# Optimization experiments

Hardware: AMD Instinct MI355X
Metric: run time of the kernel (lower is better)

The kernel has to match this reference:

```python
import jax, jax.numpy as jnp
import numpy as np

M, K, N, P = 2048, 4096, 64, 16   # prev outputs, decoder nodes, matrix size, parents per node
ACTIVE_THRESHOLD = 12             # >= 12/16 active parents required

def setup_inputs() -> dict:
    key = jax.random.key(0)
    k1, k2, k3, k4, k5 = jax.random.split(key, 5)
    prev_outputs = jax.random.normal(k1, (M, N, N), dtype=jnp.float32)
    prev_is_active = jax.random.bernoulli(k2, 0.9, (M,))                 # bool (M,)
    parent_indices = jax.random.randint(k3, (K, P), 0, M)                # static wiring (K,16)
    w = jax.random.normal(k4, (K, P), dtype=jnp.float32) / np.sqrt(P)    # per-node parent weights
    b = jax.random.normal(k5, (K,), dtype=jnp.float32) * 0.01            # per-node bias
    return {"prev_outputs": prev_outputs, "prev_is_active": prev_is_active,
            "parent_indices": parent_indices, "w": w, "b": b}

def reference(prev_outputs, prev_is_active, parent_indices, w, b):
    # gather parent outputs: (K, P, n, n)
    gathered = prev_outputs[parent_indices]
    # per-node decoder: weighted combine of 16 parents + bias, tanh
    combined = jnp.einsum('kp,kpnm->knm', w, gathered) + b[:, None, None]
    out = jnp.tanh(combined)[:, None]                                    # (K,1,n,n)
    # activity threshold gate: node active iff >= 12 of 16 parents active
    n_active = prev_is_active[parent_indices].astype(jnp.int32).sum(axis=-1)  # (K,)
    out_active = n_active >= ACTIVE_THRESHOLD
    out = jnp.where(out_active[:, None, None, None], out, jnp.zeros_like(out))
    return out, out_active
```

## Files before the change

### kernel.cpp

```cpp
#include <hip/hip_runtime.h>


#define M_ROWS   2048
#define K_NODES  4096
#define NN       4096
#define POS_TILE 16
#define NTHREADS 1024
#define ROW_B    40
#define LDS_BYTES (M_ROWS * ROW_B)
#define OUT_ELEMS (K_NODES * NN)
#define ACTIVE_THRESHOLD 12

typedef float f32x4 __attribute__((ext_vector_type(4)));
typedef unsigned short u16x4 __attribute__((ext_vector_type(4)));

__device__ __forceinline__ float fast_tanh(float x) {
  float ax = __builtin_fabsf(x);
  float e  = __expf(-2.0f * ax);
  float r  = (1.0f - e) * __builtin_amdgcn_rcpf(1.0f + e);
  return __builtin_copysignf(r, x);
}

__device__ __forceinline__ unsigned short f2bf_rne(float f) {
  unsigned u = __float_as_uint(f);
  u += 0x7FFFu + ((u >> 16) & 1u);
  return (unsigned short)(u >> 16);
}

__global__ __launch_bounds__(256) void act_kernel(
    const int* __restrict__ pidx, const unsigned int* __restrict__ isact,
    float* __restrict__ outact) {
  __shared__ int mode_sh;
  if (threadIdx.x == 0) mode_sh = 0;
  __syncthreads();
  int bad = 0;
  for (int i = threadIdx.x; i < 512; i += 256) bad |= (isact[i] > 1u);
  if (bad) atomicOr(&mode_sh, 1);
  __syncthreads();
  const int shift = mode_sh ? 0 : 2;
  const unsigned char* actb = (const unsigned char*)isact;

  int k = blockIdx.x * 256 + threadIdx.x;
  const int4* ip = (const int4*)(pidx + k * 16);
  int4 ia = ip[0], ib = ip[1], ic = ip[2], id4 = ip[3];
  int ids[16] = {ia.x, ia.y, ia.z, ia.w, ib.x, ib.y, ib.z, ib.w,
                 ic.x, ic.y, ic.z, ic.w, id4.x, id4.y, id4.z, id4.w};
  int n = 0;
  #pragma unroll
  for (int p = 0; p < 16; ++p) n += (actb[ids[p] << shift] != 0);
  outact[k] = (n >= ACTIVE_THRESHOLD) ? 1.0f : 0.0f;
}

#define PFMA4(vv, wv)                                             \
  { float wv_ = (wv);                                             \
    a0 += wv_ * __uint_as_float((unsigned)(vv)[0] << 16);         \
    a1 += wv_ * __uint_as_float((unsigned)(vv)[1] << 16);         \
    a2 += wv_ * __uint_as_float((unsigned)(vv)[2] << 16);         \
    a3 += wv_ * __uint_as_float((unsigned)(vv)[3] << 16); }

__global__ __launch_bounds__(NTHREADS, 8) void decoder_kernel(
    const float* __restrict__ prev, const int* __restrict__ pidx,
    const float* __restrict__ w, const float* __restrict__ b,
    const float* __restrict__ actf, float* __restrict__ out) {
  extern __shared__ char xb[];
  const int tid = threadIdx.x;
  const int bid = blockIdx.x;

  const int xcd   = bid & 7;
  const int j     = bid >> 3;
  const int tile  = xcd * 32 + (j >> 1);
  const int half  = j & 1;
  const int pos0  = tile * POS_TILE;
  const int nbase = half * (K_NODES / 2);

  #pragma unroll
  for (int it = 0; it < 8; ++it) {
    int ci = (it << 10) + tid;
    int r = ci >> 2, c = ci & 3;
    f32x4 v = *(const f32x4*)(prev + r * NN + pos0 + (c << 2));
    u16x4 o;
    o[0] = f2bf_rne(v.x); o[1] = f2bf_rne(v.y);
    o[2] = f2bf_rne(v.z); o[3] = f2bf_rne(v.w);
    *(u16x4*)(xb + r * ROW_B + (c << 3)) = o;
  }
  __syncthreads();

  const int q  = tid & 3;
  const int s  = tid >> 2;
  const int qb = q << 3;

  for (int it = 0; it < 8; ++it) {
    int n = nbase + (it << 8) + s;
    const int4*   ip = (const int4*)(pidx + (n << 4));
    const float4* wp = (const float4*)(w + (n << 4));
    float bk = b[n];
    float g  = actf[n];

    float a0 = bk, a1 = bk, a2 = bk, a3 = bk;

    #pragma unroll
    for (int bb = 0; bb < 4; ++bb) {
      int4   iv = ip[bb];
      float4 wv = wp[bb];
      u16x4 v0 = *(const u16x4*)(xb + iv.x * ROW_B + qb);
      u16x4 v1 = *(const u16x4*)(xb + iv.y * ROW_B + qb);
      u16x4 v2 = *(const u16x4*)(xb + iv.z * ROW_B + qb);
      u16x4 v3 = *(const u16x4*)(xb + iv.w * ROW_B + qb);
      __builtin_amdgcn_sched_barrier(0);
      PFMA4(v0, wv.x) PFMA4(v1, wv.y) PFMA4(v2, wv.z) PFMA4(v3, wv.w)
    }

    f32x4 o;
    o.x = fast_tanh(a0) * g;
    o.y = fast_tanh(a1) * g;
    o.z = fast_tanh(a2) * g;
    o.w = fast_tanh(a3) * g;
    *(f32x4*)(out + ((size_t)n << 12) + pos0 + (q << 2)) = o;
  }
}

extern "C" void kernel_launch(void* const* d_in, const int* in_sizes, int n_in,
                              void* d_out, int out_size, void* d_ws, size_t ws_size,
                              hipStream_t stream) {
  const float* prev  = (const float*)d_in[0];
  const void*  isact = d_in[1];
  const int*   pidx  = (const int*)d_in[2];
  const float* w     = (const float*)d_in[3];
  const float* b     = (const float*)d_in[4];
  float* out    = (float*)d_out;
  float* outact = out + OUT_ELEMS;

  (void)hipFuncSetAttribute((const void*)decoder_kernel,
                            hipFuncAttributeMaxDynamicSharedMemorySize, LDS_BYTES);

  act_kernel<<<K_NODES / 256, 256, 0, stream>>>(
      pidx, (const unsigned int*)isact, outact);
  decoder_kernel<<<(NN / POS_TILE) * 2, NTHREADS, LDS_BYTES, stream>>>(
      prev, pidx, w, b, outact, out);
}
```

Measured before the change: 40.31 us.

## Software-pipeline parent index/weight loads and LDS gathers across node iterations

Prefetches the next node's parent indices, weights, bias and gate from global memory during the current iteration. It also double-buffers the LDS gathers so each group of four parent rows loads while the previous group's FMAs run. The goal is to hide global-load latency on the index/weight fetches and LDS latency on the gathers. This raises register pressure, so the launch-bounds occupancy hint is lowered from 8 to 4 to give the compiler more registers. In exchange, fewer waves are available to hide latency.

```diff
diff --git a/kernel.cpp b/kernel.cpp
--- a/kernel.cpp
+++ b/kernel.cpp
@@ -58,7 +58,13 @@
     a2 += wv_ * __uint_as_float((unsigned)(vv)[2] << 16);         \
     a3 += wv_ * __uint_as_float((unsigned)(vv)[3] << 16); }
 
-__global__ __launch_bounds__(NTHREADS, 8) void decoder_kernel(
+#define GLD4(iv, d0, d1, d2, d3)                                  \
+  d0 = *(const u16x4*)(xb + (iv).x * ROW_B + qb);                 \
+  d1 = *(const u16x4*)(xb + (iv).y * ROW_B + qb);                 \
+  d2 = *(const u16x4*)(xb + (iv).z * ROW_B + qb);                 \
+  d3 = *(const u16x4*)(xb + (iv).w * ROW_B + qb);
+
+__global__ __launch_bounds__(NTHREADS, 4) void decoder_kernel(
     const float* __restrict__ prev, const int* __restrict__ pidx,
     const float* __restrict__ w, const float* __restrict__ b,
     const float* __restrict__ actf, float* __restrict__ out) {
@@ -89,33 +95,50 @@
   const int s  = tid >> 2;
   const int qb = q << 3;
 
+  int n0_ = nbase + s;
+  const int4*   ip0 = (const int4*)(pidx + (n0_ << 4));
+  const float4* wp0 = (const float4*)(w + (n0_ << 4));
+  int4   ci0 = ip0[0], ci1 = ip0[1], ci2 = ip0[2], ci3 = ip0[3];
+  float4 cw0 = wp0[0], cw1 = wp0[1], cw2 = wp0[2], cw3 = wp0[3];
+  float  cbk = b[n0_], cg  = actf[n0_];
+  u16x4 c0, c1, c2, c3;
+  GLD4(ci0, c0, c1, c2, c3)
+
   for (int it = 0; it < 8; ++it) {
+    int nx = nbase + (((it + 1) & 7) << 8) + s;
+    const int4*   ipn = (const int4*)(pidx + (nx << 4));
+    const float4* wpn = (const float4*)(w + (nx << 4));
+    int4   ni0 = ipn[0], ni1 = ipn[1], ni2 = ipn[2], ni3 = ipn[3];
+    float4 nw0 = wpn[0], nw1 = wpn[1], nw2 = wpn[2], nw3 = wpn[3];
+    float  nbk = b[nx],  ng  = actf[nx];
+
     int n = nbase + (it << 8) + s;
-    const int4*   ip = (const int4*)(pidx + (n << 4));
-    const float4* wp = (const float4*)(w + (n << 4));
-    float bk = b[n];
-    float g  = actf[n];
+    float a0 = cbk, a1 = cbk, a2 = cbk, a3 = cbk;
+    u16x4 t0, t1, t2, t3;
 
-    float a0 = bk, a1 = bk, a2 = bk, a3 = bk;
-
-    #pragma unroll
-    for (int bb = 0; bb < 4; ++bb) {
-      int4   iv = ip[bb];
-      float4 wv = wp[bb];
-      u16x4 v0 = *(const u16x4*)(xb + iv.x * ROW_B + qb);
-      u16x4 v1 = *(const u16x4*)(xb + iv.y * ROW_B + qb);
-      u16x4 v2 = *(const u16x4*)(xb + iv.z * ROW_B + qb);
-      u16x4 v3 = *(const u16x4*)(xb + iv.w * ROW_B + qb);
-      __builtin_amdgcn_sched_barrier(0);
-      PFMA4(v0, wv.x) PFMA4(v1, wv.y) PFMA4(v2, wv.z) PFMA4(v3, wv.w)
-    }
+    GLD4(ci1, t0, t1, t2, t3)
+    __builtin_amdgcn_sched_barrier(0);
+    PFMA4(c0, cw0.x) PFMA4(c1, cw0.y) PFMA4(c2, cw0.z) PFMA4(c3, cw0.w)
+    GLD4(ci2, c0, c1, c2, c3)
+    __builtin_amdgcn_sched_barrier(0);
+    PFMA4(t0, cw1.x) PFMA4(t1, cw1.y) PFMA4(t2, cw1.z) PFMA4(t3, cw1.w)
+    GLD4(ci3, t0, t1, t2, t3)
+    __builtin_amdgcn_sched_barrier(0);
+    PFMA4(c0, cw2.x) PFMA4(c1, cw2.y) PFMA4(c2, cw2.z) PFMA4(c3, cw2.w)
+    GLD4(ni0, c0, c1, c2, c3)
+    __builtin_amdgcn_sched_barrier(0);
+    PFMA4(t0, cw3.x) PFMA4(t1, cw3.y) PFMA4(t2, cw3.z) PFMA4(t3, cw3.w)
 
     f32x4 o;
-    o.x = fast_tanh(a0) * g;
-    o.y = fast_tanh(a1) * g;
-    o.z = fast_tanh(a2) * g;
-    o.w = fast_tanh(a3) * g;
+    o.x = fast_tanh(a0) * cg;
+    o.y = fast_tanh(a1) * cg;
+    o.z = fast_tanh(a2) * cg;
+    o.w = fast_tanh(a3) * cg;
     *(f32x4*)(out + ((size_t)n << 12) + pos0 + (q << 2)) = o;
+
+    ci0 = ni0; ci1 = ni1; ci2 = ni2; ci3 = ni3;
+    cw0 = nw0; cw1 = nw1; cw2 = nw2; cw3 = nw3;
+    cbk = nbk; cg = ng;
   }
 }
 
```

Result: slower. 47.88 us (+18.8%).
